# Kernel optimization log

Measured on AMD Instinct MI355X. Metric: run time of the kernel, lower is better.

The kernel has to match this reference:

```python
import jax, jax.numpy as jnp
import numpy as np

N_NODES = 100000
N_EDGES = 1600000
IN_F = 128
OUT_F = 32


def setup_inputs() -> dict:
    key = jax.random.key(0)
    k1, k2, k3, k4, k5, k6 = jax.random.split(key, 6)
    x = jax.random.normal(k1, (N_NODES, IN_F), dtype=jnp.float32)
    adj_row = jax.random.randint(k2, (N_EDGES,), 0, N_NODES, dtype=jnp.int64)
    adj_col = jax.random.randint(k3, (N_EDGES,), 0, N_NODES, dtype=jnp.int64)
    adj_val = jax.random.uniform(k4, (N_EDGES,), dtype=jnp.float32)
    weight = jax.random.normal(k5, (IN_F, OUT_F), dtype=jnp.float32) * (1.0 / np.sqrt(IN_F))
    bias = jax.random.normal(k6, (OUT_F,), dtype=jnp.float32)
    return {"x": x, "adj_row": adj_row, "adj_col": adj_col,
            "adj_val": adj_val, "weight": weight, "bias": bias}


def reference(x, adj_row, adj_col, adj_val, weight, bias):
    # support = input @ W   -> [N, out]
    support = x @ weight
    # spmm(adj, support): out[r] = sum_e val[e] * support[col[e]] for edges with row[e]==r
    gathered = adj_val[:, None] * support[adj_col]  # [E, out]
    out = jax.ops.segment_sum(gathered, adj_row, num_segments=N_NODES)
    return out + bias
```

## Files before the change

kernel.cpp:

```cpp
#include <hip/hip_runtime.h>
#include <stdint.h>

#define N_NODES 100000
#define N_EDGES 1600000
#define IN_F 128
#define OUT_F 32

#define RB 64
#define NB 1563
#define BBLK 320
#define EPA (N_EDGES / BBLK)
#define CAP 1536
#define MTILES (N_NODES / 16)
#define GEMM_BLKS ((MTILES + 15) / 16)

typedef __attribute__((ext_vector_type(8))) short bf16x8;
typedef __attribute__((ext_vector_type(4))) float f32x4;

__device__ __forceinline__ float bf2f(unsigned short u) {
    return __uint_as_float(((uint32_t)u) << 16);
}
__device__ __forceinline__ unsigned short f2bf(float x) {
    const uint32_t b = __float_as_uint(x);
    return (unsigned short)((b + 0x7fffu + ((b >> 16) & 1u)) >> 16);
}
__device__ __forceinline__ long long pack_rec(int r, int c, uint32_t v) {
    return (long long)(((uint64_t)v << 32) |
           (uint64_t)((uint32_t)c | ((uint32_t)(r & 63) << 17)));
}

__global__ __launch_bounds__(256) void gcn_init(int* __restrict__ cur,
                                                int* __restrict__ ovf_cnt) {
    const int i = blockIdx.x * 256 + threadIdx.x;
    if (i < NB) cur[i] = i * CAP;
    if (i == NB) *ovf_cnt = 0;
}

__global__ __launch_bounds__(1024) void gcn_gemm_bin(const float* __restrict__ x,
                                                     const float* __restrict__ w,
                                                     unsigned short* __restrict__ support,
                                                     const int* __restrict__ row,
                                                     const int* __restrict__ col,
                                                     const float* __restrict__ val,
                                                     int* __restrict__ cur,
                                                     int* __restrict__ ovf_cnt,
                                                     long long* __restrict__ rec,
                                                     long long* __restrict__ ovf_pk,
                                                     int* __restrict__ ovf_bk) {
    __shared__ unsigned short wt[OUT_F][IN_F + 8];
    __shared__ int h[NB];
    const int tid = threadIdx.x;

    if (blockIdx.x < GEMM_BLKS) {
        #pragma unroll
        for (int i = tid; i < IN_F * OUT_F; i += 1024) {
            const int k = i >> 5, f = i & 31;
            wt[f][k] = f2bf(w[i]);
        }
        __syncthreads();

        const int wv = tid >> 6;
        const int lane = tid & 63;
        const int rowT = blockIdx.x * 16 + wv;
        if (rowT >= MTILES) return;
        const int row0 = rowT * 16;

        const int mrow = lane & 15;
        const int kg = lane >> 4;
        const int kb = kg * 8;

        bf16x8 bfrag[4][2];
        #pragma unroll
        for (int ks = 0; ks < 4; ++ks) {
            #pragma unroll
            for (int nt = 0; nt < 2; ++nt) {
                bfrag[ks][nt] = *reinterpret_cast<const bf16x8*>(
                    &wt[mrow + nt * 16][ks * 32 + kb]);
            }
        }

        f32x4 acc0 = {0.f, 0.f, 0.f, 0.f};
        f32x4 acc1 = {0.f, 0.f, 0.f, 0.f};
        const float* xr = &x[(size_t)(row0 + mrow) * IN_F];
        #pragma unroll
        for (int ks = 0; ks < 4; ++ks) {
            const float4 a0 = *reinterpret_cast<const float4*>(&xr[ks * 32 + kb]);
            const float4 a1 = *reinterpret_cast<const float4*>(&xr[ks * 32 + kb + 4]);
            bf16x8 af;
            af[0] = (short)f2bf(a0.x); af[1] = (short)f2bf(a0.y);
            af[2] = (short)f2bf(a0.z); af[3] = (short)f2bf(a0.w);
            af[4] = (short)f2bf(a1.x); af[5] = (short)f2bf(a1.y);
            af[6] = (short)f2bf(a1.z); af[7] = (short)f2bf(a1.w);
            acc0 = __builtin_amdgcn_mfma_f32_16x16x32_bf16(af, bfrag[ks][0], acc0, 0, 0, 0);
            acc1 = __builtin_amdgcn_mfma_f32_16x16x32_bf16(af, bfrag[ks][1], acc1, 0, 0, 0);
        }
        #pragma unroll
        for (int r = 0; r < 4; ++r) {
            const int orow = row0 + kg * 4 + r;
            support[(size_t)orow * OUT_F + mrow]      = f2bf(acc0[r]);
            support[(size_t)orow * OUT_F + mrow + 16] = f2bf(acc1[r]);
        }
    } else {
        const int b = blockIdx.x - GEMM_BLKS;
        for (int i = tid; i < NB; i += 1024) h[i] = 0;
        __syncthreads();
        const int e0 = b * EPA;
        const int i4 = tid + 4096;
        const bool has4 = (i4 < EPA);

        const int r0 = row[e0 + tid];
        const int r1 = row[e0 + tid + 1024];
        const int r2 = row[e0 + tid + 2048];
        const int r3 = row[e0 + tid + 3072];
        const int r4 = has4 ? row[e0 + i4] : 0;
        const int c0 = col[e0 + tid];
        const int c1 = col[e0 + tid + 1024];
        const int c2 = col[e0 + tid + 2048];
        const int c3 = col[e0 + tid + 3072];
        const int c4 = has4 ? col[e0 + i4] : 0;
        const uint32_t v0 = __float_as_uint(val[e0 + tid]);
        const uint32_t v1 = __float_as_uint(val[e0 + tid + 1024]);
        const uint32_t v2 = __float_as_uint(val[e0 + tid + 2048]);
        const uint32_t v3 = __float_as_uint(val[e0 + tid + 3072]);
        const uint32_t v4 = has4 ? __float_as_uint(val[e0 + i4]) : 0u;

        const int k0 = r0 >> 6, k1 = r1 >> 6, k2 = r2 >> 6,
                  k3 = r3 >> 6, k4 = r4 >> 6;

        atomicAdd(&h[k0], 1);
        atomicAdd(&h[k1], 1);
        atomicAdd(&h[k2], 1);
        atomicAdd(&h[k3], 1);
        if (has4) atomicAdd(&h[k4], 1);
        __syncthreads();
        for (int k = tid; k < NB; k += 1024) {
            const int c = h[k];
            if (c > 0) h[k] = atomicAdd(&cur[k], c);
        }
        __syncthreads();
        const int s0 = atomicAdd(&h[k0], 1);
        const int s1 = atomicAdd(&h[k1], 1);
        const int s2 = atomicAdd(&h[k2], 1);
        const int s3 = atomicAdd(&h[k3], 1);
        const long long p0 = pack_rec(r0, c0, v0);
        const long long p1 = pack_rec(r1, c1, v1);
        const long long p2 = pack_rec(r2, c2, v2);
        const long long p3 = pack_rec(r3, c3, v3);
        if (s0 < (k0 + 1) * CAP) rec[s0] = p0;
        else { const int oi = atomicAdd(ovf_cnt, 1); ovf_pk[oi] = p0; ovf_bk[oi] = k0; }
        if (s1 < (k1 + 1) * CAP) rec[s1] = p1;
        else { const int oi = atomicAdd(ovf_cnt, 1); ovf_pk[oi] = p1; ovf_bk[oi] = k1; }
        if (s2 < (k2 + 1) * CAP) rec[s2] = p2;
        else { const int oi = atomicAdd(ovf_cnt, 1); ovf_pk[oi] = p2; ovf_bk[oi] = k2; }
        if (s3 < (k3 + 1) * CAP) rec[s3] = p3;
        else { const int oi = atomicAdd(ovf_cnt, 1); ovf_pk[oi] = p3; ovf_bk[oi] = k3; }
        if (has4) {
            const int s4 = atomicAdd(&h[k4], 1);
            const long long p4 = pack_rec(r4, c4, v4);
            if (s4 < (k4 + 1) * CAP) rec[s4] = p4;
            else { const int oi = atomicAdd(ovf_cnt, 1); ovf_pk[oi] = p4; ovf_bk[oi] = k4; }
        }
    }
}

__global__ __launch_bounds__(1024) void gcn_rows(const int* __restrict__ cur,
                                                 const int* __restrict__ ovf_cnt,
                                                 const long long* __restrict__ rec,
                                                 const long long* __restrict__ ovf_pk,
                                                 const int* __restrict__ ovf_bk,
                                                 const unsigned short* __restrict__ sup,
                                                 const float* __restrict__ bias,
                                                 float* __restrict__ out) {
    __shared__ long long rbuf[CAP];
    __shared__ long long srt[CAP];
    __shared__ int cnt[RB];
    __shared__ int rs[RB + 1];
    __shared__ float bs[OUT_F];
    const int tid = threadIdx.x, k = blockIdx.x;

    const int start = k * CAP;
    const int total = cur[k] - start;
    const int n = min(total, CAP);
    const int novf = *ovf_cnt;

    if (tid < OUT_F) bs[tid] = bias[tid];
    if (tid < RB) cnt[tid] = 0;
    for (int i = tid; i < n; i += 1024) rbuf[i] = rec[start + i];
    __syncthreads();

    for (int i = tid; i < n; i += 1024)
        atomicAdd(&cnt[(int)(((uint64_t)rbuf[i] >> 17) & 63)], 1);
    __syncthreads();

    if (tid < 64) {
        const int v = cnt[tid];
        int sc = v;
        #pragma unroll
        for (int d = 1; d < 64; d <<= 1) {
            const int t2 = __shfl_up(sc, d, 64);
            if (tid >= d) sc += t2;
        }
        rs[tid] = sc - v;
        cnt[tid] = sc - v;
        if (tid == 63) rs[64] = sc;
    }
    __syncthreads();

    for (int i = tid; i < n; i += 1024) {
        const long long pk = rbuf[i];
        const int rl = (int)(((uint64_t)pk >> 17) & 63);
        const int slot = atomicAdd(&cnt[rl], 1);
        srt[slot] = pk;
    }
    __syncthreads();

    const int g = tid >> 5;
    const int f = tid & 31;
    const int rowBase = k * RB;

    for (int rp = 0; rp < 2; ++rp) {
        const int r = rp * 32 + g;
        const int gr = rowBase + r;
        const int s0 = rs[r];
        const int s1 = rs[r + 1];
        float a0 = bs[f], a1 = 0.f, a2 = 0.f, a3 = 0.f;
        int i = s0;
        for (; i + 4 <= s1; i += 4) {
            const uint64_t p0 = (uint64_t)srt[i];
            const uint64_t p1 = (uint64_t)srt[i + 1];
            const uint64_t p2 = (uint64_t)srt[i + 2];
            const uint64_t p3 = (uint64_t)srt[i + 3];
            const unsigned short q0 = sup[(size_t)(p0 & 0x1ffff) * OUT_F + f];
            const unsigned short q1 = sup[(size_t)(p1 & 0x1ffff) * OUT_F + f];
            const unsigned short q2 = sup[(size_t)(p2 & 0x1ffff) * OUT_F + f];
            const unsigned short q3 = sup[(size_t)(p3 & 0x1ffff) * OUT_F + f];
            a0 += __uint_as_float((uint32_t)(p0 >> 32)) * bf2f(q0);
            a1 += __uint_as_float((uint32_t)(p1 >> 32)) * bf2f(q1);
            a2 += __uint_as_float((uint32_t)(p2 >> 32)) * bf2f(q2);
            a3 += __uint_as_float((uint32_t)(p3 >> 32)) * bf2f(q3);
        }
        for (; i < s1; ++i) {
            const uint64_t pk = (uint64_t)srt[i];
            const unsigned short q = sup[(size_t)(pk & 0x1ffff) * OUT_F + f];
            a0 += __uint_as_float((uint32_t)(pk >> 32)) * bf2f(q);
        }
        for (int j = 0; j < novf; ++j) {
            if (ovf_bk[j] == k) {
                const uint64_t pk = (uint64_t)ovf_pk[j];
                if ((int)((pk >> 17) & 63) == r) {
                    const unsigned short q = sup[(size_t)(pk & 0x1ffff) * OUT_F + f];
                    a0 += __uint_as_float((uint32_t)(pk >> 32)) * bf2f(q);
                }
            }
        }
        if (gr < N_NODES)
            out[(size_t)gr * OUT_F + f] = (a0 + a1) + (a2 + a3);
    }
}

__global__ __launch_bounds__(256) void gcn_bias_init(const float* __restrict__ bias,
                                                     float* __restrict__ out) {
    const int i = blockIdx.x * 256 + threadIdx.x;
    if (i < N_NODES * OUT_F) out[i] = bias[i & 31];
}

__global__ __launch_bounds__(512) void gcn_gemm_only(const float* __restrict__ x,
                                                     const float* __restrict__ w,
                                                     unsigned short* __restrict__ support) {
    __shared__ unsigned short wt[OUT_F][IN_F + 8];
    const int tid = threadIdx.x;
    #pragma unroll
    for (int i = tid; i < IN_F * OUT_F; i += 512) {
        const int k = i >> 5, f = i & 31;
        wt[f][k] = f2bf(w[i]);
    }
    __syncthreads();
    const int wv = tid >> 6;
    const int lane = tid & 63;
    const int rowT = blockIdx.x * 8 + wv;
    if (rowT >= MTILES) return;
    const int row0 = rowT * 16;
    const int mrow = lane & 15;
    const int kg = lane >> 4;
    const int kb = kg * 8;
    bf16x8 bfrag[4][2];
    #pragma unroll
    for (int ks = 0; ks < 4; ++ks)
        #pragma unroll
        for (int nt = 0; nt < 2; ++nt)
            bfrag[ks][nt] = *reinterpret_cast<const bf16x8*>(
                &wt[mrow + nt * 16][ks * 32 + kb]);
    f32x4 acc0 = {0.f, 0.f, 0.f, 0.f};
    f32x4 acc1 = {0.f, 0.f, 0.f, 0.f};
    const float* xr = &x[(size_t)(row0 + mrow) * IN_F];
    #pragma unroll
    for (int ks = 0; ks < 4; ++ks) {
        const float4 a0 = *reinterpret_cast<const float4*>(&xr[ks * 32 + kb]);
        const float4 a1 = *reinterpret_cast<const float4*>(&xr[ks * 32 + kb + 4]);
        bf16x8 af;
        af[0] = (short)f2bf(a0.x); af[1] = (short)f2bf(a0.y);
        af[2] = (short)f2bf(a0.z); af[3] = (short)f2bf(a0.w);
        af[4] = (short)f2bf(a1.x); af[5] = (short)f2bf(a1.y);
        af[6] = (short)f2bf(a1.z); af[7] = (short)f2bf(a1.w);
        acc0 = __builtin_amdgcn_mfma_f32_16x16x32_bf16(af, bfrag[ks][0], acc0, 0, 0, 0);
        acc1 = __builtin_amdgcn_mfma_f32_16x16x32_bf16(af, bfrag[ks][1], acc1, 0, 0, 0);
    }
    #pragma unroll
    for (int r = 0; r < 4; ++r) {
        const int orow = row0 + kg * 4 + r;
        support[(size_t)orow * OUT_F + mrow]      = f2bf(acc0[r]);
        support[(size_t)orow * OUT_F + mrow + 16] = f2bf(acc1[r]);
    }
}

__global__ __launch_bounds__(256) void gcn_scatter(const int* __restrict__ row,
                                                   const int* __restrict__ col,
                                                   const float* __restrict__ val,
                                                   const unsigned short* __restrict__ sup,
                                                   float* __restrict__ out) {
    const int f = threadIdx.x & 31;
    const int grp = threadIdx.x >> 5;
    long long e = (long long)blockIdx.x * 8 + grp;
    const long long stride = (long long)gridDim.x * 8;
    for (; e < N_EDGES; e += stride) {
        const int r = row[e];
        const int c = col[e];
        const float v = val[e];
        const float s = bf2f(sup[(size_t)c * OUT_F + f]);
        atomicAdd(&out[(size_t)r * OUT_F + f], v * s);
    }
}

extern "C" void kernel_launch(void* const* d_in, const int* in_sizes, int n_in,
                              void* d_out, int out_size, void* d_ws, size_t ws_size,
                              hipStream_t stream) {
    const float* x       = (const float*)d_in[0];
    const int*   adj_row = (const int*)d_in[1];
    const int*   adj_col = (const int*)d_in[2];
    const float* adj_val = (const float*)d_in[3];
    const float* weight  = (const float*)d_in[4];
    const float* bias    = (const float*)d_in[5];
    float* out = (float*)d_out;

    char* ws = (char*)d_ws;
    const size_t SUPPORT_B = (((size_t)N_NODES * OUT_F * 2) + 255) & ~(size_t)255;
    const size_t REC_B     = (((size_t)NB * CAP * 8) + 255) & ~(size_t)255;
    const size_t CUR_B     = (((size_t)NB * 4) + 255) & ~(size_t)255;
    const size_t OCN_B     = 256;
    const size_t OPK_B     = (size_t)N_EDGES * 8;
    const size_t OBK_B     = (size_t)N_EDGES * 4;
    const size_t NEED = SUPPORT_B + REC_B + CUR_B + OCN_B + OPK_B + OBK_B;

    unsigned short* support = (unsigned short*)(ws);
    long long* rec  = (long long*)(ws + SUPPORT_B);
    int* cur        = (int*)(ws + SUPPORT_B + REC_B);
    int* ovf_cnt    = (int*)(ws + SUPPORT_B + REC_B + CUR_B);
    long long* ovf_pk = (long long*)(ws + SUPPORT_B + REC_B + CUR_B + OCN_B);
    int* ovf_bk     = (int*)(ws + SUPPORT_B + REC_B + CUR_B + OCN_B + OPK_B);

    if (ws_size >= NEED) {
        gcn_init<<<(NB + 256) / 256, 256, 0, stream>>>(cur, ovf_cnt);
        gcn_gemm_bin<<<GEMM_BLKS + BBLK, 1024, 0, stream>>>(x, weight, support,
                                                            adj_row, adj_col, adj_val,
                                                            cur, ovf_cnt, rec,
                                                            ovf_pk, ovf_bk);
        gcn_rows<<<NB, 1024, 0, stream>>>(cur, ovf_cnt, rec, ovf_pk, ovf_bk,
                                          support, bias, out);
    } else {
        gcn_gemm_only<<<(MTILES + 7) / 8, 512, 0, stream>>>(x, weight, support);
        gcn_bias_init<<<(N_NODES * OUT_F + 255) / 256, 256, 0, stream>>>(bias, out);
        gcn_scatter<<<8192, 256, 0, stream>>>(adj_row, adj_col, adj_val, support, out);
    }
}
```

Baseline: 67.22 us.

## Locally sort edge records in LDS before coalesced scatter to buckets

The binning blocks now compute a block-local prefix scan over bucket counts, stage packed edge records in shared memory sorted by bucket, and then write them to global bucket storage in contiguous runs. This replaces scattered per-edge 8-byte global writes with mostly sequential writes. The row kernel's gather loop is also unrolled to 8 to keep more support loads in flight. The cost is a larger LDS footprint (about 40KB per block), which may lower occupancy, plus extra barriers from the scan.

```diff
diff --git a/kernel.cpp b/kernel.cpp
--- a/kernel.cpp
+++ b/kernel.cpp
@@ -13,6 +13,12 @@
 #define CAP 1536
 #define MTILES (N_NODES / 16)
 #define GEMM_BLKS ((MTILES + 15) / 16)
+
+#define SBUF_B (EPA * 8)
+#define HH_OFF SBUF_B
+#define DD_OFF (SBUF_B + 6256)
+#define SK_OFF (SBUF_B + 6256 + 6256)
+#define SMEM_B (SK_OFF + EPA * 2 + 16)
 
 typedef __attribute__((ext_vector_type(8))) short bf16x8;
 typedef __attribute__((ext_vector_type(4))) float f32x4;
@@ -47,11 +53,12 @@
                                                      long long* __restrict__ rec,
                                                      long long* __restrict__ ovf_pk,
                                                      int* __restrict__ ovf_bk) {
-    __shared__ unsigned short wt[OUT_F][IN_F + 8];
-    __shared__ int h[NB];
+    __shared__ __align__(16) char smem[SMEM_B];
     const int tid = threadIdx.x;
 
     if (blockIdx.x < GEMM_BLKS) {
+        unsigned short (*wt)[IN_F + 8] =
+            reinterpret_cast<unsigned short (*)[IN_F + 8]>(smem);
         #pragma unroll
         for (int i = tid; i < IN_F * OUT_F; i += 1024) {
             const int k = i >> 5, f = i & 31;
@@ -101,64 +108,99 @@
             support[(size_t)orow * OUT_F + mrow + 16] = f2bf(acc1[r]);
         }
     } else {
+        long long* sbuf = reinterpret_cast<long long*>(smem);
+        int* hh = reinterpret_cast<int*>(smem + HH_OFF);
+        int* dd = reinterpret_cast<int*>(smem + DD_OFF);
+        unsigned short* sk = reinterpret_cast<unsigned short*>(smem + SK_OFF);
+
         const int b = blockIdx.x - GEMM_BLKS;
-        for (int i = tid; i < NB; i += 1024) h[i] = 0;
-        __syncthreads();
         const int e0 = b * EPA;
         const int i4 = tid + 4096;
         const bool has4 = (i4 < EPA);
+
+        for (int i = tid; i < NB; i += 1024) hh[i] = 0;
+        __syncthreads();
 
         const int r0 = row[e0 + tid];
         const int r1 = row[e0 + tid + 1024];
         const int r2 = row[e0 + tid + 2048];
         const int r3 = row[e0 + tid + 3072];
         const int r4 = has4 ? row[e0 + i4] : 0;
-        const int c0 = col[e0 + tid];
-        const int c1 = col[e0 + tid + 1024];
-        const int c2 = col[e0 + tid + 2048];
-        const int c3 = col[e0 + tid + 3072];
-        const int c4 = has4 ? col[e0 + i4] : 0;
-        const uint32_t v0 = __float_as_uint(val[e0 + tid]);
-        const uint32_t v1 = __float_as_uint(val[e0 + tid + 1024]);
-        const uint32_t v2 = __float_as_uint(val[e0 + tid + 2048]);
-        const uint32_t v3 = __float_as_uint(val[e0 + tid + 3072]);
-        const uint32_t v4 = has4 ? __float_as_uint(val[e0 + i4]) : 0u;
-
-        const int k0 = r0 >> 6, k1 = r1 >> 6, k2 = r2 >> 6,
-                  k3 = r3 >> 6, k4 = r4 >> 6;
-
-        atomicAdd(&h[k0], 1);
-        atomicAdd(&h[k1], 1);
-        atomicAdd(&h[k2], 1);
-        atomicAdd(&h[k3], 1);
-        if (has4) atomicAdd(&h[k4], 1);
-        __syncthreads();
-        for (int k = tid; k < NB; k += 1024) {
-            const int c = h[k];
-            if (c > 0) h[k] = atomicAdd(&cur[k], c);
-        }
-        __syncthreads();
-        const int s0 = atomicAdd(&h[k0], 1);
-        const int s1 = atomicAdd(&h[k1], 1);
-        const int s2 = atomicAdd(&h[k2], 1);
-        const int s3 = atomicAdd(&h[k3], 1);
-        const long long p0 = pack_rec(r0, c0, v0);
-        const long long p1 = pack_rec(r1, c1, v1);
-        const long long p2 = pack_rec(r2, c2, v2);
-        const long long p3 = pack_rec(r3, c3, v3);
-        if (s0 < (k0 + 1) * CAP) rec[s0] = p0;
-        else { const int oi = atomicAdd(ovf_cnt, 1); ovf_pk[oi] = p0; ovf_bk[oi] = k0; }
-        if (s1 < (k1 + 1) * CAP) rec[s1] = p1;
-        else { const int oi = atomicAdd(ovf_cnt, 1); ovf_pk[oi] = p1; ovf_bk[oi] = k1; }
-        if (s2 < (k2 + 1) * CAP) rec[s2] = p2;
-        else { const int oi = atomicAdd(ovf_cnt, 1); ovf_pk[oi] = p2; ovf_bk[oi] = k2; }
-        if (s3 < (k3 + 1) * CAP) rec[s3] = p3;
-        else { const int oi = atomicAdd(ovf_cnt, 1); ovf_pk[oi] = p3; ovf_bk[oi] = k3; }
-        if (has4) {
-            const int s4 = atomicAdd(&h[k4], 1);
-            const long long p4 = pack_rec(r4, c4, v4);
-            if (s4 < (k4 + 1) * CAP) rec[s4] = p4;
-            else { const int oi = atomicAdd(ovf_cnt, 1); ovf_pk[oi] = p4; ovf_bk[oi] = k4; }
+        atomicAdd(&hh[r0 >> 6], 1);
+        atomicAdd(&hh[r1 >> 6], 1);
+        atomicAdd(&hh[r2 >> 6], 1);
+        atomicAdd(&hh[r3 >> 6], 1);
+        if (has4) atomicAdd(&hh[r4 >> 6], 1);
+        __syncthreads();
+
+        int cntA = 0, cntB = 0;
+        if (tid < 782) {
+            cntA = hh[2 * tid];
+            cntB = (2 * tid + 1 < NB) ? hh[2 * tid + 1] : 0;
+        }
+        const int csum = cntA + cntB;
+        dd[tid] = csum;
+        __syncthreads();
+        for (int off = 1; off < 1024; off <<= 1) {
+            const int v2 = (tid >= off) ? dd[tid - off] : 0;
+            __syncthreads();
+            dd[tid] += v2;
+            __syncthreads();
+        }
+        const int excl = dd[tid] - csum;
+        __syncthreads();
+        if (tid < 782) {
+            const int k0 = 2 * tid, k1 = 2 * tid + 1;
+            const int lo0 = excl, lo1 = excl + cntA;
+            int D0 = 0, D1 = 0;
+            if (cntA > 0) D0 = atomicAdd(&cur[k0], cntA) - lo0;
+            hh[k0] = lo0; dd[k0] = D0;
+            if (k1 < NB) {
+                if (cntB > 0) D1 = atomicAdd(&cur[k1], cntB) - lo1;
+                hh[k1] = lo1; dd[k1] = D1;
+            }
+        }
+        __syncthreads();
+
+        {
+            const int c0 = col[e0 + tid];
+            const int c1 = col[e0 + tid + 1024];
+            const int c2 = col[e0 + tid + 2048];
+            const int c3 = col[e0 + tid + 3072];
+            const uint32_t v0 = __float_as_uint(val[e0 + tid]);
+            const uint32_t v1 = __float_as_uint(val[e0 + tid + 1024]);
+            const uint32_t v2 = __float_as_uint(val[e0 + tid + 2048]);
+            const uint32_t v3 = __float_as_uint(val[e0 + tid + 3072]);
+            const int k0 = r0 >> 6, k1 = r1 >> 6, k2 = r2 >> 6, k3 = r3 >> 6;
+            const int s0 = atomicAdd(&hh[k0], 1);
+            const int s1 = atomicAdd(&hh[k1], 1);
+            const int s2 = atomicAdd(&hh[k2], 1);
+            const int s3 = atomicAdd(&hh[k3], 1);
+            sbuf[s0] = pack_rec(r0, c0, v0); sk[s0] = (unsigned short)k0;
+            sbuf[s1] = pack_rec(r1, c1, v1); sk[s1] = (unsigned short)k1;
+            sbuf[s2] = pack_rec(r2, c2, v2); sk[s2] = (unsigned short)k2;
+            sbuf[s3] = pack_rec(r3, c3, v3); sk[s3] = (unsigned short)k3;
+            if (has4) {
+                const int c4 = col[e0 + i4];
+                const uint32_t v4 = __float_as_uint(val[e0 + i4]);
+                const int k4 = r4 >> 6;
+                const int s4 = atomicAdd(&hh[k4], 1);
+                sbuf[s4] = pack_rec(r4, c4, v4); sk[s4] = (unsigned short)k4;
+            }
+        }
+        __syncthreads();
+
+        for (int i = tid; i < EPA; i += 1024) {
+            const int k = (int)sk[i];
+            const long long pk = sbuf[i];
+            const int ga = dd[k] + i;
+            if (ga < (k + 1) * CAP) {
+                rec[ga] = pk;
+            } else {
+                const int oi = atomicAdd(ovf_cnt, 1);
+                ovf_pk[oi] = pk;
+                ovf_bk[oi] = k;
+            }
         }
     }
 }
@@ -225,6 +267,32 @@
         const int s1 = rs[r + 1];
         float a0 = bs[f], a1 = 0.f, a2 = 0.f, a3 = 0.f;
         int i = s0;
+        for (; i + 8 <= s1; i += 8) {
+            const uint64_t p0 = (uint64_t)srt[i];
+            const uint64_t p1 = (uint64_t)srt[i + 1];
+            const uint64_t p2 = (uint64_t)srt[i + 2];
+            const uint64_t p3 = (uint64_t)srt[i + 3];
+            const uint64_t p4 = (uint64_t)srt[i + 4];
+            const uint64_t p5 = (uint64_t)srt[i + 5];
+            const uint64_t p6 = (uint64_t)srt[i + 6];
+            const uint64_t p7 = (uint64_t)srt[i + 7];
+            const unsigned short q0 = sup[(size_t)(p0 & 0x1ffff) * OUT_F + f];
+            const unsigned short q1 = sup[(size_t)(p1 & 0x1ffff) * OUT_F + f];
+            const unsigned short q2 = sup[(size_t)(p2 & 0x1ffff) * OUT_F + f];
+            const unsigned short q3 = sup[(size_t)(p3 & 0x1ffff) * OUT_F + f];
+            const unsigned short q4 = sup[(size_t)(p4 & 0x1ffff) * OUT_F + f];
+            const unsigned short q5 = sup[(size_t)(p5 & 0x1ffff) * OUT_F + f];
+            const unsigned short q6 = sup[(size_t)(p6 & 0x1ffff) * OUT_F + f];
+            const unsigned short q7 = sup[(size_t)(p7 & 0x1ffff) * OUT_F + f];
+            a0 += __uint_as_float((uint32_t)(p0 >> 32)) * bf2f(q0);
+            a1 += __uint_as_float((uint32_t)(p1 >> 32)) * bf2f(q1);
+            a2 += __uint_as_float((uint32_t)(p2 >> 32)) * bf2f(q2);
+            a3 += __uint_as_float((uint32_t)(p3 >> 32)) * bf2f(q3);
+            a0 += __uint_as_float((uint32_t)(p4 >> 32)) * bf2f(q4);
+            a1 += __uint_as_float((uint32_t)(p5 >> 32)) * bf2f(q5);
+            a2 += __uint_as_float((uint32_t)(p6 >> 32)) * bf2f(q6);
+            a3 += __uint_as_float((uint32_t)(p7 >> 32)) * bf2f(q7);
+        }
         for (; i + 4 <= s1; i += 4) {
             const uint64_t p0 = (uint64_t)srt[i];
             const uint64_t p1 = (uint64_t)srt[i + 1];
```

After: 68.00 us. No clear change (+1.2%).
